# Performance work log

Measured on AMD Instinct MI355X. Metric: run time of the kernel, lower is better.

## Reference

```python
import jax, jax.numpy as jnp
import numpy as np

NUM_CATEGORIES = 32
INPUT_DIM = 1536
HIDDEN_DIM = 1024
OUTPUT_DIM = 1024
B, T = 128, 32


def setup_inputs() -> dict:
    key = jax.random.key(0)
    k_x, k_cat, k_w1, k_w2 = jax.random.split(key, 4)
    x = jax.random.normal(k_x, (B, T, INPUT_DIM), dtype=jnp.float32)
    cat_ids = jax.random.randint(k_cat, (B,), 0, NUM_CATEGORIES)
    # CategorySpecificLinear params: W ~ 0.02*randn, b = zeros
    W1 = 0.02 * jax.random.normal(k_w1, (NUM_CATEGORIES, INPUT_DIM, HIDDEN_DIM), dtype=jnp.float32)
    b1 = jnp.zeros((NUM_CATEGORIES, HIDDEN_DIM), dtype=jnp.float32)
    W2 = 0.02 * jax.random.normal(k_w2, (NUM_CATEGORIES, HIDDEN_DIM, OUTPUT_DIM), dtype=jnp.float32)
    b2 = jnp.zeros((NUM_CATEGORIES, OUTPUT_DIM), dtype=jnp.float32)
    return {"x": x, "cat_ids": cat_ids, "W1": W1, "b1": b1, "W2": W2, "b2": b2}


def _cat_linear(x, W, b, cat_ids):
    # x: (B, T, D_in); W: (C, D_in, D_out); b: (C, D_out)
    # torch: bmm(x, W[cat_ids]) + b[cat_ids].unsqueeze(1)
    return jnp.einsum("btd,bdh->bth", x, W[cat_ids]) + b[cat_ids][:, None, :]


def reference(x, cat_ids, W1, b1, W2, b2):
    # CategorySpecificMLP.forward
    hidden = jax.nn.relu(_cat_linear(x, W1, b1, cat_ids))  # (B, T, H)
    return _cat_linear(hidden, W2, b2, cat_ids)            # (B, T, O)
```

## Files before the change

### kernel.cpp

```cpp
#include <hip/hip_runtime.h>
#include <hip/hip_bf16.h>
#include <stdint.h>

#define NCAT 32
#define DIN  1536
#define DMID 1024
#define NB   128
#define TT   32

#define BM 128
#define BN 128
#define BK 32
#define LDA 40
#define MAXG 56

typedef __attribute__((ext_vector_type(8))) short short8;
typedef __attribute__((ext_vector_type(4))) float f32x4;

static __device__ __forceinline__ unsigned int pk2bf(float lo, float hi) {
  unsigned short a = __builtin_bit_cast(unsigned short, __float2bfloat16(lo));
  unsigned short b = __builtin_bit_cast(unsigned short, __float2bfloat16(hi));
  return ((unsigned int)b << 16) | (unsigned int)a;
}

__global__ void build_groups(const int* __restrict__ cat_ids, int* __restrict__ wsi) {
  __shared__ int cats[NB];
  __shared__ int cnt[NCAT];
  __shared__ int off[NCAT];
  int t = threadIdx.x;
  cats[t] = cat_ids[t];
  __syncthreads();
  if (t < NCAT) {
    int n = 0;
    for (int b = 0; b < NB; b++) n += (cats[b] == t);
    cnt[t] = n;
  }
  __syncthreads();
  if (t == 0) {
    int acc = 0;
    for (int c = 0; c < NCAT; c++) { off[c] = acc; acc += cnt[c]; }
  }
  __syncthreads();
  if (t < NCAT) {
    int o = off[t];
    for (int b = 0; b < NB; b++)
      if (cats[b] == t) wsi[o++] = b;
  }
  if (t == 0) {
    int g = 0;
    for (int c = 0; c < NCAT; c++) {
      int n = cnt[c], o = off[c];
      for (int j = 0; j < n; j += 4) {
        wsi[132 + g * 4 + 0] = c;
        wsi[132 + g * 4 + 1] = o + j;
        wsi[132 + g * 4 + 2] = (n - j) < 4 ? (n - j) : 4;
        g++;
      }
    }
    wsi[128] = g;
  }
}

template <int LAYER>
__global__ __launch_bounds__(256, 2)
void mlp_gemm(const void* __restrict__ Ain, const float* __restrict__ W,
              const float* __restrict__ bias, const int* __restrict__ wsi,
              void* __restrict__ Out, int K) {
  int gid = blockIdx.y;
  if (gid >= wsi[128]) return;
  const int cat   = wsi[132 + gid * 4 + 0];
  const int start = wsi[132 + gid * 4 + 1];
  const int cnt   = wsi[132 + gid * 4 + 2];
  const int n0    = blockIdx.x * BN;

  __shared__ unsigned short As[BM * LDA];
  __shared__ unsigned short Bs[4 * 128 * 8];

  const int tid  = threadIdx.x;
  const int lane = tid & 63;
  const int w    = tid >> 6;

  const int arow  = tid >> 1;
  const int khalf = (tid & 1) * 16;
  const int lb    = arow >> 5;
  const int tok   = arow & 31;
  const int lbc   = lb < (cnt - 1) ? lb : (cnt - 1);
  const int batch = wsi[start + lbc];
  const long grow = (long)(batch * TT + tok);

  const int bn = 2 * lane;
  const float* Wg = W + (size_t)cat * (size_t)K * 1024 + n0;

  f32x4 acc[4][4];
#pragma unroll
  for (int i = 0; i < 4; i++)
#pragma unroll
    for (int j = 0; j < 4; j++) acc[i][j] = (f32x4){0.f, 0.f, 0.f, 0.f};

  const int wm = (w >> 1) * 64;
  const int wn = (w & 1) * 64;
  const int kg = lane >> 4;
  const int c16 = lane & 15;

  for (int k0 = 0; k0 < K; k0 += BK) {
    uint4 aw0, aw1;
    if constexpr (LAYER == 1) {
      const float* ap = (const float*)Ain + grow * (long)K + k0 + khalf;
      float4 a0 = *(const float4*)(ap + 0);
      float4 a1 = *(const float4*)(ap + 4);
      float4 a2 = *(const float4*)(ap + 8);
      float4 a3 = *(const float4*)(ap + 12);
      aw0 = make_uint4(pk2bf(a0.x, a0.y), pk2bf(a0.z, a0.w),
                       pk2bf(a1.x, a1.y), pk2bf(a1.z, a1.w));
      aw1 = make_uint4(pk2bf(a2.x, a2.y), pk2bf(a2.z, a2.w),
                       pk2bf(a3.x, a3.y), pk2bf(a3.z, a3.w));
    } else {
      const uint4* ap = (const uint4*)((const unsigned short*)Ain + grow * (long)K + k0 + khalf);
      aw0 = ap[0];
      aw1 = ap[1];
    }
    float2 bv[8];
    {
      const float* bp = Wg + (size_t)(k0 + w * 8) * 1024 + bn;
#pragma unroll
      for (int r = 0; r < 8; r++) bv[r] = *(const float2*)(bp + (size_t)r * 1024);
    }
    uint4 bw0 = make_uint4(pk2bf(bv[0].x, bv[1].x), pk2bf(bv[2].x, bv[3].x),
                           pk2bf(bv[4].x, bv[5].x), pk2bf(bv[6].x, bv[7].x));
    uint4 bw1 = make_uint4(pk2bf(bv[0].y, bv[1].y), pk2bf(bv[2].y, bv[3].y),
                           pk2bf(bv[4].y, bv[5].y), pk2bf(bv[6].y, bv[7].y));

    __syncthreads();

    *(uint4*)&As[arow * LDA + khalf]     = aw0;
    *(uint4*)&As[arow * LDA + khalf + 8] = aw1;
    {
      int nA = bn, nB = bn + 1;
      int sA = (w * 128 + (nA ^ ((nA >> 3) & 1))) * 8;
      int sB = (w * 128 + (nB ^ ((nB >> 3) & 1))) * 8;
      *(uint4*)&Bs[sA] = bw0;
      *(uint4*)&Bs[sB] = bw1;
    }
    __syncthreads();

    short8 afrag[4], bfrag[4];
#pragma unroll
    for (int i = 0; i < 4; i++)
      afrag[i] = *(const short8*)&As[(wm + i * 16 + c16) * LDA + kg * 8];
#pragma unroll
    for (int j = 0; j < 4; j++) {
      int n = wn + j * 16 + c16;
      int slot = (kg * 128 + (n ^ ((n >> 3) & 1))) * 8;
      bfrag[j] = *(const short8*)&Bs[slot];
    }
#pragma unroll
    for (int i = 0; i < 4; i++)
#pragma unroll
      for (int j = 0; j < 4; j++)
        acc[i][j] = __builtin_amdgcn_mfma_f32_16x16x32_bf16(afrag[i], bfrag[j], acc[i][j], 0, 0, 0);
  }

  const int rquad = (lane >> 4) * 4;
#pragma unroll
  for (int i = 0; i < 4; i++) {
#pragma unroll
    for (int j = 0; j < 4; j++) {
      int gcol = n0 + wn + j * 16 + c16;
      float bb = bias[cat * 1024 + gcol];
#pragma unroll
      for (int r = 0; r < 4; r++) {
        int lrow = wm + i * 16 + rquad + r;
        int lb2 = lrow >> 5;
        if (lb2 < cnt) {
          int b2 = wsi[start + lb2];
          long orow = (long)(b2 * TT + (lrow & 31));
          float v = acc[i][j][r] + bb;
          if constexpr (LAYER == 1) {
            v = fmaxf(v, 0.f);
            ((unsigned short*)Out)[orow * DMID + gcol] =
                __builtin_bit_cast(unsigned short, __float2bfloat16(v));
          } else {
            ((float*)Out)[orow * 1024 + gcol] = v;
          }
        }
      }
    }
  }
}

extern "C" void kernel_launch(void* const* d_in, const int* in_sizes, int n_in,
                              void* d_out, int out_size, void* d_ws, size_t ws_size,
                              hipStream_t stream) {
  const float* x       = (const float*)d_in[0];
  const int*   cat_ids = (const int*)d_in[1];
  const float* W1      = (const float*)d_in[2];
  const float* b1      = (const float*)d_in[3];
  const float* W2      = (const float*)d_in[4];
  const float* b2      = (const float*)d_in[5];
  float* out = (float*)d_out;

  int* wsi = (int*)d_ws;
  unsigned short* hidden = (unsigned short*)((char*)d_ws + 8192);

  build_groups<<<dim3(1), dim3(128), 0, stream>>>(cat_ids, wsi);
  mlp_gemm<1><<<dim3(DMID / BN, MAXG), dim3(256), 0, stream>>>(
      (const void*)x, W1, b1, wsi, (void*)hidden, DIN);
  mlp_gemm<2><<<dim3(1024 / BN, MAXG), dim3(256), 0, stream>>>(
      (const void*)hidden, W2, b2, wsi, (void*)out, DMID);
}
```

Measured before the change: 456.4 us.

## Halve N tile and prefetch next K tile into registers during MFMA

```diff
diff --git a/kernel.cpp b/kernel.cpp
--- a/kernel.cpp
+++ b/kernel.cpp
@@ -9,7 +9,7 @@
 #define TT   32
 
 #define BM 128
-#define BN 128
+#define BN 64
 #define BK 32
 #define LDA 40
 #define MAXG 56
@@ -62,7 +62,7 @@
 }
 
 template <int LAYER>
-__global__ __launch_bounds__(256, 2)
+__global__ __launch_bounds__(256)
 void mlp_gemm(const void* __restrict__ Ain, const float* __restrict__ W,
               const float* __restrict__ bias, const int* __restrict__ wsi,
               void* __restrict__ Out, int K) {
@@ -74,7 +74,7 @@
   const int n0    = blockIdx.x * BN;
 
   __shared__ unsigned short As[BM * LDA];
-  __shared__ unsigned short Bs[4 * 128 * 8];
+  __shared__ unsigned short Bs[4 * BN * 8];
 
   const int tid  = threadIdx.x;
   const int lane = tid & 63;
@@ -88,83 +88,90 @@
   const int batch = wsi[start + lbc];
   const long grow = (long)(batch * TT + tok);
 
-  const int bn = 2 * lane;
-  const float* Wg = W + (size_t)cat * (size_t)K * 1024 + n0;
-
-  f32x4 acc[4][4];
+  const float* Wcol = W + (size_t)cat * (size_t)K * 1024 + n0 + lane;
+
+  f32x4 acc[4][2];
 #pragma unroll
   for (int i = 0; i < 4; i++)
 #pragma unroll
-    for (int j = 0; j < 4; j++) acc[i][j] = (f32x4){0.f, 0.f, 0.f, 0.f};
-
-  const int wm = (w >> 1) * 64;
-  const int wn = (w & 1) * 64;
-  const int kg = lane >> 4;
+    for (int j = 0; j < 2; j++) acc[i][j] = (f32x4){0.f, 0.f, 0.f, 0.f};
+
+  const int wm  = (w >> 1) * 64;
+  const int wn  = (w & 1) * 32;
+  const int kg  = lane >> 4;
   const int c16 = lane & 15;
 
-  for (int k0 = 0; k0 < K; k0 += BK) {
-    uint4 aw0, aw1;
+  auto load_tile = [&](int k0, float4 ar[4], uint4& ah0, uint4& ah1, float br[8]) {
     if constexpr (LAYER == 1) {
       const float* ap = (const float*)Ain + grow * (long)K + k0 + khalf;
-      float4 a0 = *(const float4*)(ap + 0);
-      float4 a1 = *(const float4*)(ap + 4);
-      float4 a2 = *(const float4*)(ap + 8);
-      float4 a3 = *(const float4*)(ap + 12);
-      aw0 = make_uint4(pk2bf(a0.x, a0.y), pk2bf(a0.z, a0.w),
-                       pk2bf(a1.x, a1.y), pk2bf(a1.z, a1.w));
-      aw1 = make_uint4(pk2bf(a2.x, a2.y), pk2bf(a2.z, a2.w),
-                       pk2bf(a3.x, a3.y), pk2bf(a3.z, a3.w));
+      ar[0] = *(const float4*)(ap + 0);
+      ar[1] = *(const float4*)(ap + 4);
+      ar[2] = *(const float4*)(ap + 8);
+      ar[3] = *(const float4*)(ap + 12);
     } else {
       const uint4* ap = (const uint4*)((const unsigned short*)Ain + grow * (long)K + k0 + khalf);
-      aw0 = ap[0];
-      aw1 = ap[1];
-    }
-    float2 bv[8];
-    {
-      const float* bp = Wg + (size_t)(k0 + w * 8) * 1024 + bn;
-#pragma unroll
-      for (int r = 0; r < 8; r++) bv[r] = *(const float2*)(bp + (size_t)r * 1024);
-    }
-    uint4 bw0 = make_uint4(pk2bf(bv[0].x, bv[1].x), pk2bf(bv[2].x, bv[3].x),
-                           pk2bf(bv[4].x, bv[5].x), pk2bf(bv[6].x, bv[7].x));
-    uint4 bw1 = make_uint4(pk2bf(bv[0].y, bv[1].y), pk2bf(bv[2].y, bv[3].y),
-                           pk2bf(bv[4].y, bv[5].y), pk2bf(bv[6].y, bv[7].y));
-
+      ah0 = ap[0];
+      ah1 = ap[1];
+    }
+    const float* bp = Wcol + (size_t)(k0 + w * 8) * 1024;
+#pragma unroll
+    for (int r = 0; r < 8; r++) br[r] = bp[(size_t)r * 1024];
+  };
+
+  auto store_tile = [&](const float4 ar[4], const uint4& ah0, const uint4& ah1,
+                        const float br[8]) {
+    if constexpr (LAYER == 1) {
+      uint4 aw0 = make_uint4(pk2bf(ar[0].x, ar[0].y), pk2bf(ar[0].z, ar[0].w),
+                             pk2bf(ar[1].x, ar[1].y), pk2bf(ar[1].z, ar[1].w));
+      uint4 aw1 = make_uint4(pk2bf(ar[2].x, ar[2].y), pk2bf(ar[2].z, ar[2].w),
+                             pk2bf(ar[3].x, ar[3].y), pk2bf(ar[3].z, ar[3].w));
+      *(uint4*)&As[arow * LDA + khalf]     = aw0;
+      *(uint4*)&As[arow * LDA + khalf + 8] = aw1;
+    } else {
+      *(uint4*)&As[arow * LDA + khalf]     = ah0;
+      *(uint4*)&As[arow * LDA + khalf + 8] = ah1;
+    }
+    uint4 bw = make_uint4(pk2bf(br[0], br[1]), pk2bf(br[2], br[3]),
+                          pk2bf(br[4], br[5]), pk2bf(br[6], br[7]));
+    *(uint4*)&Bs[(w * BN + lane) * 8] = bw;
+  };
+
+  float4 arC[4]; uint4 ah0C, ah1C; float brC[8];
+  load_tile(0, arC, ah0C, ah1C, brC);
+
+  for (int k0 = 0; k0 < K; k0 += BK) {
     __syncthreads();
-
-    *(uint4*)&As[arow * LDA + khalf]     = aw0;
-    *(uint4*)&As[arow * LDA + khalf + 8] = aw1;
-    {
-      int nA = bn, nB = bn + 1;
-      int sA = (w * 128 + (nA ^ ((nA >> 3) & 1))) * 8;
-      int sB = (w * 128 + (nB ^ ((nB >> 3) & 1))) * 8;
-      *(uint4*)&Bs[sA] = bw0;
-      *(uint4*)&Bs[sB] = bw1;
-    }
+    store_tile(arC, ah0C, ah1C, brC);
     __syncthreads();
 
-    short8 afrag[4], bfrag[4];
+    float4 arN[4]; uint4 ah0N, ah1N; float brN[8];
+    if (k0 + BK < K) load_tile(k0 + BK, arN, ah0N, ah1N, brN);
+
+    short8 afrag[4], bfrag[2];
 #pragma unroll
     for (int i = 0; i < 4; i++)
       afrag[i] = *(const short8*)&As[(wm + i * 16 + c16) * LDA + kg * 8];
 #pragma unroll
-    for (int j = 0; j < 4; j++) {
-      int n = wn + j * 16 + c16;
-      int slot = (kg * 128 + (n ^ ((n >> 3) & 1))) * 8;
-      bfrag[j] = *(const short8*)&Bs[slot];
-    }
+    for (int j = 0; j < 2; j++)
+      bfrag[j] = *(const short8*)&Bs[(kg * BN + wn + j * 16 + c16) * 8];
 #pragma unroll
     for (int i = 0; i < 4; i++)
 #pragma unroll
-      for (int j = 0; j < 4; j++)
+      for (int j = 0; j < 2; j++)
         acc[i][j] = __builtin_amdgcn_mfma_f32_16x16x32_bf16(afrag[i], bfrag[j], acc[i][j], 0, 0, 0);
+
+#pragma unroll
+    for (int i = 0; i < 4; i++) arC[i] = arN[i];
+    ah0C = ah0N; ah1C = ah1N;
+#pragma unroll
+    for (int r = 0; r < 8; r++) brC[r] = brN[r];
   }
 
   const int rquad = (lane >> 4) * 4;
 #pragma unroll
   for (int i = 0; i < 4; i++) {
 #pragma unroll
-    for (int j = 0; j < 4; j++) {
+    for (int j = 0; j < 2; j++) {
       int gcol = n0 + wn + j * 16 + c16;
       float bb = bias[cat * 1024 + gcol];
 #pragma unroll
@@ -203,7 +210,7 @@
   unsigned short* hidden = (unsigned short*)((char*)d_ws + 8192);
 
   build_groups<<<dim3(1), dim3(128), 0, stream>>>(cat_ids, wsi);
-  mlp_gemm<1><<<dim3(DMID / BN, MAXG), dim3(256), 0, stream>>>(
+  mlp_gemm<1><<<dim3(1024 / BN, MAXG), dim3(256), 0, stream>>>(
       (const void*)x, W1, b1, wsi, (void*)hidden, DIN);
   mlp_gemm<2><<<dim3(1024 / BN, MAXG), dim3(256), 0, stream>>>(
       (const void*)hidden, W2, b2, wsi, (void*)out, DMID);
```

Result: faster. 444.8 us (-2.6%).
